# Optimization experiments

Hardware: AMD Instinct MI355X
Metric: run time of the kernel (lower is better)

## Reference

```python
import jax, jax.numpy as jnp
import numpy as np

N_NODES = 100000
N_EDGES = 3200000
D_IN = 256
D_OUT = 256


def setup_inputs() -> dict:
    key = jax.random.key(0)
    k1, k2, k3, k4, k5 = jax.random.split(key, 5)
    inputs = jax.random.normal(k1, (N_NODES, D_IN), dtype=jnp.float32)
    adj_row = jax.random.randint(k2, (N_EDGES,), 0, N_NODES, dtype=jnp.int32)
    adj_col = jax.random.randint(k3, (N_EDGES,), 0, N_NODES, dtype=jnp.int32)
    adj_val = jax.random.uniform(k4, (N_EDGES,), dtype=jnp.float32)
    # xavier-uniform init for weight, zeros for bias (as in reset_parameters)
    limit = float(np.sqrt(6.0 / (D_IN + D_OUT)))
    weight = jax.random.uniform(k5, (D_IN, D_OUT), dtype=jnp.float32,
                                minval=-limit, maxval=limit)
    bias = jnp.zeros((D_OUT,), dtype=jnp.float32)
    return {"inputs": inputs, "adj_row": adj_row, "adj_col": adj_col,
            "adj_val": adj_val, "weight": weight, "bias": bias}


def reference(inputs, adj_row, adj_col, adj_val, weight, bias) -> jnp.ndarray:
    # support = X @ W  -> [N, D_OUT]
    support = inputs @ weight
    # SpMM: out[r] = sum_{e: row[e]==r} val[e] * support[col[e]]
    gathered = support[adj_col] * adj_val[:, None]          # [E, D_OUT]
    output = jax.ops.segment_sum(gathered, adj_row, num_segments=N_NODES)
    return output + bias
```

## Files before the change

### kernel.cpp

```cpp
#include <hip/hip_runtime.h>

#define N_NODES 100000
#define N_EDGES 3200000
#define D 256
#define NBLK ((N_NODES + 255) / 256)
#define GEMM_TILES (N_NODES / 32)
#define GEMM_BLOCKS ((GEMM_TILES + 3) / 4)
#define HIST_BLOCKS (N_EDGES / 256)
#define ZERO_BLOCKS NBLK
#define WSH_BLOCKS 32

#define RPB 16
#define NB_BUCKETS (N_NODES / RPB)
#define P2_CAP 4096

using u16 = unsigned short;
using u32 = unsigned int;

typedef __attribute__((ext_vector_type(8))) short bf16x8;
typedef __attribute__((ext_vector_type(4))) float f32x4;

__device__ inline u16 f2bf(float f) {
    u32 x = __builtin_bit_cast(u32, f);
    return (u16)((x + 0x7FFFu + ((x >> 16) & 1u)) >> 16);
}
__device__ inline float bf2f(u16 u) {
    return __builtin_bit_cast(float, (u32)u << 16);
}

__global__ __launch_bounds__(256) void prep_kernel(
    const float* __restrict__ W, u16* __restrict__ Wf, int* __restrict__ cnt)
{
    if (blockIdx.x < ZERO_BLOCKS) {
        const int i = blockIdx.x * 256 + threadIdx.x;
        if (i < N_NODES) cnt[i] = 0;
        return;
    }
    const int t = (blockIdx.x - ZERO_BLOCKS) * 256 + threadIdx.x;
    const int kt = t >> 10;
    const int nt = (t >> 6) & 15;
    const int lane = t & 63;
    const int kbase = kt * 32 + ((lane >> 4) * 8);
    const int n = nt * 16 + (lane & 15);
    u16 frag[8];
    #pragma unroll
    for (int j = 0; j < 8; ++j)
        frag[j] = f2bf(W[(size_t)(kbase + j) * D + n]);
    #pragma unroll
    for (int j = 0; j < 8; ++j)
        Wf[(size_t)t * 8 + j] = frag[j];
}

__global__ __launch_bounds__(256) void gemm_hist_kernel(
    const float* __restrict__ X, const u16* __restrict__ Wf,
    u16* __restrict__ S, const int* __restrict__ row, int* __restrict__ cnt)
{
    if (blockIdx.x >= GEMM_BLOCKS) {
        const int e = (blockIdx.x - GEMM_BLOCKS) * 256 + threadIdx.x;
        atomicAdd(&cnt[row[e]], 1);
        return;
    }
    const int lane = threadIdx.x & 63;
    const int tile = blockIdx.x * 4 + (threadIdx.x >> 6);
    if (tile >= GEMM_TILES) return;
    const int row0 = tile * 32;
    const int m = lane & 15;
    const int quad = lane >> 4;

    f32x4 acc0[16], acc1[16];
    #pragma unroll
    for (int t = 0; t < 16; ++t) {
        acc0[t] = (f32x4){0.f, 0.f, 0.f, 0.f};
        acc1[t] = (f32x4){0.f, 0.f, 0.f, 0.f};
    }

    const float* xA = X + (size_t)(row0 + m) * D + quad * 8;
    const float* xB = X + (size_t)(row0 + 16 + m) * D + quad * 8;
    const bf16x8* __restrict__ Bf = (const bf16x8*)Wf;

    for (int k0 = 0; k0 < 8; ++k0) {
        const float4 a0l = *(const float4*)(xA + k0 * 32);
        const float4 a0h = *(const float4*)(xA + k0 * 32 + 4);
        const float4 a1l = *(const float4*)(xB + k0 * 32);
        const float4 a1h = *(const float4*)(xB + k0 * 32 + 4);
        bf16x8 a0, a1;
        a0[0] = (short)f2bf(a0l.x); a0[1] = (short)f2bf(a0l.y);
        a0[2] = (short)f2bf(a0l.z); a0[3] = (short)f2bf(a0l.w);
        a0[4] = (short)f2bf(a0h.x); a0[5] = (short)f2bf(a0h.y);
        a0[6] = (short)f2bf(a0h.z); a0[7] = (short)f2bf(a0h.w);
        a1[0] = (short)f2bf(a1l.x); a1[1] = (short)f2bf(a1l.y);
        a1[2] = (short)f2bf(a1l.z); a1[3] = (short)f2bf(a1l.w);
        a1[4] = (short)f2bf(a1h.x); a1[5] = (short)f2bf(a1h.y);
        a1[6] = (short)f2bf(a1h.z); a1[7] = (short)f2bf(a1h.w);

        const bf16x8* bp = Bf + (size_t)k0 * 1024 + lane;
        #pragma unroll
        for (int g = 0; g < 4; ++g) {
            const bf16x8 b0 = bp[g * 256 + 0];
            const bf16x8 b1 = bp[g * 256 + 64];
            const bf16x8 b2 = bp[g * 256 + 128];
            const bf16x8 b3 = bp[g * 256 + 192];
            acc0[g*4+0] = __builtin_amdgcn_mfma_f32_16x16x32_bf16(a0, b0, acc0[g*4+0], 0, 0, 0);
            acc1[g*4+0] = __builtin_amdgcn_mfma_f32_16x16x32_bf16(a1, b0, acc1[g*4+0], 0, 0, 0);
            acc0[g*4+1] = __builtin_amdgcn_mfma_f32_16x16x32_bf16(a0, b1, acc0[g*4+1], 0, 0, 0);
            acc1[g*4+1] = __builtin_amdgcn_mfma_f32_16x16x32_bf16(a1, b1, acc1[g*4+1], 0, 0, 0);
            acc0[g*4+2] = __builtin_amdgcn_mfma_f32_16x16x32_bf16(a0, b2, acc0[g*4+2], 0, 0, 0);
            acc1[g*4+2] = __builtin_amdgcn_mfma_f32_16x16x32_bf16(a1, b2, acc1[g*4+2], 0, 0, 0);
            acc0[g*4+3] = __builtin_amdgcn_mfma_f32_16x16x32_bf16(a0, b3, acc0[g*4+3], 0, 0, 0);
            acc1[g*4+3] = __builtin_amdgcn_mfma_f32_16x16x32_bf16(a1, b3, acc1[g*4+3], 0, 0, 0);
        }
    }

    #pragma unroll
    for (int nt = 0; nt < 16; ++nt) {
        #pragma unroll
        for (int i = 0; i < 4; ++i) {
            S[(size_t)(row0 + quad * 4 + i) * D + nt * 16 + m]      = f2bf(acc0[nt][i]);
            S[(size_t)(row0 + 16 + quad * 4 + i) * D + nt * 16 + m] = f2bf(acc1[nt][i]);
        }
    }
}

__global__ __launch_bounds__(256) void blocksum_kernel(
    const int* __restrict__ cnt, int* __restrict__ bsum)
{
    __shared__ int sh[4];
    const int i = blockIdx.x * 256 + threadIdx.x;
    int x = (i < N_NODES) ? cnt[i] : 0;
    #pragma unroll
    for (int off = 32; off > 0; off >>= 1) x += __shfl_xor(x, off);
    if ((threadIdx.x & 63) == 0) sh[threadIdx.x >> 6] = x;
    __syncthreads();
    if (threadIdx.x == 0) bsum[blockIdx.x] = sh[0] + sh[1] + sh[2] + sh[3];
}

__global__ __launch_bounds__(512) void bscan_kernel(
    const int* __restrict__ bsum, int* __restrict__ boff, int* __restrict__ starts)
{
    __shared__ int wsum[8];
    const int tid = threadIdx.x, lane = tid & 63, wv = tid >> 6;
    const int c = (tid < NBLK) ? bsum[tid] : 0;
    int x = c;
    #pragma unroll
    for (int off = 1; off < 64; off <<= 1) {
        int y = __shfl_up(x, off);
        if (lane >= off) x += y;
    }
    if (lane == 63) wsum[wv] = x;
    __syncthreads();
    if (tid == 0) {
        int run = 0;
        #pragma unroll
        for (int w = 0; w < 8; ++w) { int t = wsum[w]; wsum[w] = run; run += t; }
        starts[N_NODES] = N_EDGES;
    }
    __syncthreads();
    if (tid < NBLK) boff[tid] = x - c + wsum[wv];
}

__global__ __launch_bounds__(256) void localscan_kernel(
    const int* __restrict__ cnt, const int* __restrict__ boff,
    int* __restrict__ starts, int* __restrict__ bcur)
{
    __shared__ int wsum[4];
    const int tid = threadIdx.x, lane = tid & 63, wv = tid >> 6;
    const int i = blockIdx.x * 256 + tid;
    const int c = (i < N_NODES) ? cnt[i] : 0;
    int x = c;
    #pragma unroll
    for (int off = 1; off < 64; off <<= 1) {
        int y = __shfl_up(x, off);
        if (lane >= off) x += y;
    }
    if (lane == 63) wsum[wv] = x;
    __syncthreads();
    if (tid == 0) {
        int run = 0;
        #pragma unroll
        for (int w = 0; w < 4; ++w) { int t = wsum[w]; wsum[w] = run; run += t; }
    }
    __syncthreads();
    const int excl = x - c + wsum[wv] + boff[blockIdx.x];
    if (i < N_NODES) {
        starts[i] = excl;
        if ((i & (RPB - 1)) == 0) bcur[i / RPB] = excl;
    }
}

__global__ __launch_bounds__(256) void binplace_kernel(
    const int* __restrict__ row, const int* __restrict__ col,
    const float* __restrict__ val, int* __restrict__ bcur,
    uint2* __restrict__ pce)
{
    const int e = blockIdx.x * 256 + threadIdx.x;
    const int r = row[e];
    const u32 c = (u32)col[e];
    const float v = val[e];
    const int pos = atomicAdd(&bcur[r / RPB], 1);
    pce[pos] = make_uint2(c | ((u32)(r & (RPB - 1)) << 17),
                          __builtin_bit_cast(u32, v));
}

__global__ __launch_bounds__(256) void bucketsort_kernel(
    const int* __restrict__ starts, uint2* __restrict__ pce)
{
    __shared__ uint2 ent[P2_CAP];
    __shared__ int rbase[RPB + 1];
    __shared__ int rcnt[RPB];
    const int b = blockIdx.x;
    const int tid = threadIdx.x;
    if (tid <= RPB) rbase[tid] = starts[b * RPB + tid];
    if (tid < RPB) rcnt[tid] = 0;
    __syncthreads();
    const int base = rbase[0];
    const int n = rbase[RPB] - base;
    for (int i = tid; i < n; i += 256) ent[i] = pce[base + i];
    __syncthreads();
    for (int i = tid; i < n; i += 256) {
        const uint2 e = ent[i];
        const int rlow = (int)((e.x >> 17) & (u32)(RPB - 1));
        const int rank = atomicAdd(&rcnt[rlow], 1);
        pce[rbase[rlow] + rank] = make_uint2(e.x & 0x1FFFFu, e.y);
    }
}

__global__ __launch_bounds__(256) void reduce_kernel(
    const u16* __restrict__ S, const int* __restrict__ starts,
    const uint2* __restrict__ pce, const float* __restrict__ bias,
    float* __restrict__ out)
{
    const int lane = threadIdx.x & 63;
    const int r = blockIdx.x * 4 + (threadIdx.x >> 6);
    const int s0 = starts[r];
    const int s1 = starts[r + 1];

    const ushort4* __restrict__ S4 = (const ushort4*)S;
    float4 acc = make_float4(0.f, 0.f, 0.f, 0.f);

    for (int base = s0; base < s1; base += 64) {
        const int n = min(64, s1 - base);
        uint2 pr = make_uint2(0u, 0u);
        if (lane < n) pr = pce[base + lane];
        const int c = (int)pr.x;
        const float v = __builtin_bit_cast(float, pr.y);

        int i = 0;
        for (; i + 8 <= n; i += 8) {
            int cc[8]; float vv[8]; ushort4 s[8];
            #pragma unroll
            for (int u = 0; u < 8; ++u) {
                cc[u] = __shfl(c, i + u);
                vv[u] = __shfl(v, i + u);
            }
            #pragma unroll
            for (int u = 0; u < 8; ++u)
                s[u] = S4[(size_t)cc[u] * 64 + lane];
            #pragma unroll
            for (int u = 0; u < 8; ++u) {
                acc.x += vv[u] * bf2f(s[u].x);
                acc.y += vv[u] * bf2f(s[u].y);
                acc.z += vv[u] * bf2f(s[u].z);
                acc.w += vv[u] * bf2f(s[u].w);
            }
        }
        for (; i < n; ++i) {
            const int c0 = __shfl(c, i);
            const float v0 = __shfl(v, i);
            const ushort4 a0 = S4[(size_t)c0 * 64 + lane];
            acc.x += v0 * bf2f(a0.x);
            acc.y += v0 * bf2f(a0.y);
            acc.z += v0 * bf2f(a0.z);
            acc.w += v0 * bf2f(a0.w);
        }
    }

    const float4 b4 = ((const float4*)bias)[lane];
    acc.x += b4.x; acc.y += b4.y; acc.z += b4.z; acc.w += b4.w;
    ((float4*)out)[(size_t)r * 64 + lane] = acc;
}

extern "C" void kernel_launch(void* const* d_in, const int* in_sizes, int n_in,
                              void* d_out, int out_size, void* d_ws, size_t ws_size,
                              hipStream_t stream) {
    const float* X    = (const float*)d_in[0];
    const int*   row  = (const int*)d_in[1];
    const int*   col  = (const int*)d_in[2];
    const float* val  = (const float*)d_in[3];
    const float* W    = (const float*)d_in[4];
    const float* bias = (const float*)d_in[5];
    float* out = (float*)d_out;

    char* ws = (char*)d_ws;
    u16*   Sx     = (u16*)ws;
    int*   starts = (int*)(ws + 51200000);
    uint2* pce    = (uint2*)(ws + 51600064);
    int*   cnt    = (int*)(ws + 51600064);
    u16*   Wf     = (u16*)(ws + 77200064);
    int*   bsum   = (int*)(ws + 77331136);
    int*   boff   = (int*)(ws + 77333184);
    int*   bcur   = (int*)(ws + 77335232);

    prep_kernel<<<ZERO_BLOCKS + WSH_BLOCKS, 256, 0, stream>>>(W, Wf, cnt);

    gemm_hist_kernel<<<GEMM_BLOCKS + HIST_BLOCKS, 256, 0, stream>>>(X, Wf, Sx, row, cnt);

    blocksum_kernel<<<NBLK, 256, 0, stream>>>(cnt, bsum);
    bscan_kernel<<<1, 512, 0, stream>>>(bsum, boff, starts);
    localscan_kernel<<<NBLK, 256, 0, stream>>>(cnt, boff, starts, bcur);

    binplace_kernel<<<N_EDGES / 256, 256, 0, stream>>>(row, col, val, bcur, pce);
    bucketsort_kernel<<<NB_BUCKETS, 256, 0, stream>>>(starts, pce);

    reduce_kernel<<<N_NODES / 4, 256, 0, stream>>>(Sx, starts, pce, bias, out);
}
```

Measured before the change: 723.7 us.

## Split support matrix into two column planes and run SpMM reduce per plane

The GEMM now writes the bf16 support matrix as two planes of 128 columns each, and the reduce kernel is launched twice, once per plane. Each plane holds 25.6 MB, so it is more likely to stay resident in L2/MALL cache during the random gather. In exchange, the edge list (pce, starts) is read twice, there is an extra kernel launch, and each lane now does 4-byte loads instead of 8-byte loads.

```diff
diff --git a/kernel.cpp b/kernel.cpp
--- a/kernel.cpp
+++ b/kernel.cpp
@@ -113,10 +113,12 @@
 
     #pragma unroll
     for (int nt = 0; nt < 16; ++nt) {
+        u16* Sp = S + (size_t)(nt >> 3) * ((size_t)N_NODES * 128);
+        const int cip = (nt & 7) * 16 + m;
         #pragma unroll
         for (int i = 0; i < 4; ++i) {
-            S[(size_t)(row0 + quad * 4 + i) * D + nt * 16 + m]      = f2bf(acc0[nt][i]);
-            S[(size_t)(row0 + 16 + quad * 4 + i) * D + nt * 16 + m] = f2bf(acc1[nt][i]);
+            Sp[(size_t)(row0 + quad * 4 + i) * 128 + cip]      = f2bf(acc0[nt][i]);
+            Sp[(size_t)(row0 + 16 + quad * 4 + i) * 128 + cip] = f2bf(acc1[nt][i]);
         }
     }
 }
@@ -227,15 +229,16 @@
 __global__ __launch_bounds__(256) void reduce_kernel(
     const u16* __restrict__ S, const int* __restrict__ starts,
     const uint2* __restrict__ pce, const float* __restrict__ bias,
-    float* __restrict__ out)
+    float* __restrict__ out, int plane)
 {
     const int lane = threadIdx.x & 63;
     const int r = blockIdx.x * 4 + (threadIdx.x >> 6);
     const int s0 = starts[r];
     const int s1 = starts[r + 1];
 
-    const ushort4* __restrict__ S4 = (const ushort4*)S;
-    float4 acc = make_float4(0.f, 0.f, 0.f, 0.f);
+    const u32* __restrict__ Sp =
+        (const u32*)(S + (size_t)plane * ((size_t)N_NODES * 128));
+    float2 acc = make_float2(0.f, 0.f);
 
     for (int base = s0; base < s1; base += 64) {
         const int n = min(64, s1 - base);
@@ -246,7 +249,7 @@
 
         int i = 0;
         for (; i + 8 <= n; i += 8) {
-            int cc[8]; float vv[8]; ushort4 s[8];
+            int cc[8]; float vv[8]; u32 s[8];
             #pragma unroll
             for (int u = 0; u < 8; ++u) {
                 cc[u] = __shfl(c, i + u);
@@ -254,29 +257,25 @@
             }
             #pragma unroll
             for (int u = 0; u < 8; ++u)
-                s[u] = S4[(size_t)cc[u] * 64 + lane];
+                s[u] = Sp[(size_t)cc[u] * 64 + lane];
             #pragma unroll
             for (int u = 0; u < 8; ++u) {
-                acc.x += vv[u] * bf2f(s[u].x);
-                acc.y += vv[u] * bf2f(s[u].y);
-                acc.z += vv[u] * bf2f(s[u].z);
-                acc.w += vv[u] * bf2f(s[u].w);
+                acc.x += vv[u] * bf2f((u16)(s[u] & 0xFFFFu));
+                acc.y += vv[u] * bf2f((u16)(s[u] >> 16));
             }
         }
         for (; i < n; ++i) {
             const int c0 = __shfl(c, i);
             const float v0 = __shfl(v, i);
-            const ushort4 a0 = S4[(size_t)c0 * 64 + lane];
-            acc.x += v0 * bf2f(a0.x);
-            acc.y += v0 * bf2f(a0.y);
-            acc.z += v0 * bf2f(a0.z);
-            acc.w += v0 * bf2f(a0.w);
+            const u32 a0 = Sp[(size_t)c0 * 64 + lane];
+            acc.x += v0 * bf2f((u16)(a0 & 0xFFFFu));
+            acc.y += v0 * bf2f((u16)(a0 >> 16));
         }
     }
 
-    const float4 b4 = ((const float4*)bias)[lane];
-    acc.x += b4.x; acc.y += b4.y; acc.z += b4.z; acc.w += b4.w;
-    ((float4*)out)[(size_t)r * 64 + lane] = acc;
+    const float2 b2 = ((const float2*)bias)[plane * 64 + lane];
+    acc.x += b2.x; acc.y += b2.y;
+    ((float2*)out)[(size_t)r * 128 + plane * 64 + lane] = acc;
 }
 
 extern "C" void kernel_launch(void* const* d_in, const int* in_sizes, int n_in,
@@ -311,5 +310,6 @@
     binplace_kernel<<<N_EDGES / 256, 256, 0, stream>>>(row, col, val, bcur, pce);
     bucketsort_kernel<<<NB_BUCKETS, 256, 0, stream>>>(starts, pce);
 
-    reduce_kernel<<<N_NODES / 4, 256, 0, stream>>>(Sx, starts, pce, bias, out);
-}
+    reduce_kernel<<<N_NODES / 4, 256, 0, stream>>>(Sx, starts, pce, bias, out, 0);
+    reduce_kernel<<<N_NODES / 4, 256, 0, stream>>>(Sx, starts, pce, bias, out, 1);
+}
```

Measured after the change: 717.7 us. Within noise of the previous version (-0.8%).
